# Performance work log

Measured on AMD Instinct MI355X. Metric: run time of the kernel, lower is better.

Reference implementation:

```python
import jax, jax.numpy as jnp
import numpy as np

D_MODEL = 1024
NUM_HEADS = 16
HEAD_DIM = D_MODEL // NUM_HEADS
SEQ_LEN = 2048
THETA = 10000.0


def setup_inputs() -> dict:
    key = jax.random.key(0)
    ks = jax.random.split(key, 9)
    s = 1.0 / np.sqrt(D_MODEL)
    inp = {
        "x": jax.random.normal(ks[0], (2, SEQ_LEN, D_MODEL), dtype=jnp.float32),
        "Wq": jax.random.uniform(ks[1], (D_MODEL, D_MODEL), jnp.float32, -s, s),
        "bq": jax.random.uniform(ks[2], (D_MODEL,), jnp.float32, -s, s),
        "Wk": jax.random.uniform(ks[3], (D_MODEL, D_MODEL), jnp.float32, -s, s),
        "bk": jax.random.uniform(ks[4], (D_MODEL,), jnp.float32, -s, s),
        "Wv": jax.random.uniform(ks[5], (D_MODEL, D_MODEL), jnp.float32, -s, s),
        "bv": jax.random.uniform(ks[6], (D_MODEL,), jnp.float32, -s, s),
        "Wo": jax.random.uniform(ks[7], (D_MODEL, D_MODEL), jnp.float32, -s, s),
        "bo": jax.random.uniform(ks[8], (D_MODEL,), jnp.float32, -s, s),
    }
    return inp


def _rope_cos_sin(seq_len, dim, theta):
    inv_freq = 1.0 / theta ** (jnp.arange(0, dim, 2, dtype=jnp.float32) / dim)  # [dim/2]
    t = jnp.arange(seq_len, dtype=jnp.float32)
    freqs = jnp.outer(t, inv_freq)  # [S, dim/2]
    return jnp.cos(freqs), jnp.sin(freqs)


def _apply_rope(x, cos, sin):
    # x: [B, H, S, head_dim]; interleaved complex pairs (even, odd)
    x2 = x.reshape(*x.shape[:-1], -1, 2)  # [B,H,S,hd/2,2]
    xe, xo = x2[..., 0], x2[..., 1]
    c = cos[None, None, :, :]
    s = sin[None, None, :, :]
    oe = xe * c - xo * s
    oo = xe * s + xo * c
    return jnp.stack([oe, oo], axis=-1).reshape(x.shape)


def reference(x, Wq, bq, Wk, bk, Wv, bv, Wo, bo):
    B, S, D = x.shape
    H, hd = NUM_HEADS, HEAD_DIM
    q = x @ Wq.T + bq
    k = x @ Wk.T + bk
    v = x @ Wv.T + bv
    # [B, H, S, hd]
    q = q.reshape(B, S, H, hd).transpose(0, 2, 1, 3)
    k = k.reshape(B, S, H, hd).transpose(0, 2, 1, 3)
    v = v.reshape(B, S, H, hd).transpose(0, 2, 1, 3)
    cos, sin = _rope_cos_sin(S, hd, THETA)
    q = _apply_rope(q, cos, sin)
    k = _apply_rope(k, cos, sin)
    scores = jnp.einsum("bhqd,bhkd->bhqk", q, k) / jnp.sqrt(jnp.float32(hd))
    causal = jnp.triu(jnp.ones((S, S), dtype=bool), k=1)
    scores = jnp.where(causal[None, None, :, :], -jnp.inf, scores)
    attn = jax.nn.softmax(scores, axis=-1)
    out = jnp.einsum("bhqk,bhkd->bhqd", attn, v)
    out = out.transpose(0, 2, 1, 3).reshape(B, S, D)
    return out @ Wo.T + bo
```

## Files before the change

kernel.cpp:

```cpp
#include <hip/hip_runtime.h>
#include <hip/hip_bf16.h>

#define S_LEN 2048
#define DM 1024
#define NH 16
#define HD 64
#define M_ROWS 4096
#define LOG2E 1.4426950408889634f
#define MASKVAL -1.0e4f
#define QSCALE 0.18033688011112042f

typedef __attribute__((ext_vector_type(8))) short short8;
typedef __attribute__((ext_vector_type(2))) float f32x2;
typedef __attribute__((ext_vector_type(4))) float f32x4;
typedef __attribute__((ext_vector_type(16))) float f32x16;

__device__ inline ushort f2b(float f) {
  union { float f; unsigned u; } v; v.f = f;
  unsigned r = v.u + 0x7fffu + ((v.u >> 16) & 1u);
  return (ushort)(r >> 16);
}

__device__ inline float b2f(ushort u) {
  union { unsigned u; float f; } v; v.u = ((unsigned)u) << 16; return v.f;
}

__device__ inline unsigned pk_bf16(float a, float b) {
  __hip_bfloat162 h = __float22bfloat162_rn(make_float2(a, b));
  union { __hip_bfloat162 h; unsigned u; } v; v.h = h;
  return v.u;
}

__device__ inline float fexp2(float x) { return __builtin_amdgcn_exp2f(x); }

__device__ inline void gl_lds16(const void* g, void* l) {
  __builtin_amdgcn_global_load_lds(
      (const __attribute__((address_space(1))) void*)g,
      (__attribute__((address_space(3))) void*)l, 16, 0, 0);
}

__global__ __launch_bounds__(256) void cast_rope_kernel(
    const float* __restrict__ x, const float* __restrict__ Wq, const float* __restrict__ Wk,
    const float* __restrict__ Wv, const float* __restrict__ Wo,
    ushort* __restrict__ xb, ushort* __restrict__ Wqb, ushort* __restrict__ Wkb,
    ushort* __restrict__ Wvb, ushort* __restrict__ Wob,
    float* __restrict__ ropeC, float* __restrict__ ropeS) {
  const int bid = blockIdx.x;
  if (bid >= 8192) {
    int idx = (bid - 8192) * 256 + threadIdx.x;
    int s = idx >> 5, i = idx & 31;
    float inv = exp2f(-(float)i * (13.287712379549449f / 32.0f));
    float a = (float)s * inv;
    ropeC[idx] = cosf(a);
    ropeS[idx] = sinf(a);
    return;
  }
  int i = bid * 256 + threadIdx.x;
  int r = i >> 18, off = i & 0x3FFFF;
  const float4* s;
  uint2* d;
  switch (r) {
    case 0: case 1: case 2: case 3: s = (const float4*)x + i;  d = (uint2*)xb + i;  break;
    case 4: s = (const float4*)Wq + off; d = (uint2*)Wqb + off; break;
    case 5: s = (const float4*)Wk + off; d = (uint2*)Wkb + off; break;
    case 6: s = (const float4*)Wv + off; d = (uint2*)Wvb + off; break;
    default: s = (const float4*)Wo + off; d = (uint2*)Wob + off; break;
  }
  float4 v = *s;
  uint2 o;
  o.x = pk_bf16(v.x, v.y);
  o.y = pk_bf16(v.z, v.w);
  *d = o;
}

__global__ __launch_bounds__(256) void gemm_qkv_kernel(const ushort* __restrict__ xb,
    const ushort* __restrict__ Wqb, const ushort* __restrict__ Wkb, const ushort* __restrict__ Wvb,
    const float* __restrict__ bq, const float* __restrict__ bk, const float* __restrict__ bv,
    const float* __restrict__ ropeC, const float* __restrict__ ropeS,
    ushort* __restrict__ qb, ushort* __restrict__ kb, ushort* __restrict__ vT) {
  __shared__ ushort lds[17408];
  ushort* As = lds;
  ushort* Bs = lds + 8192;
  const int z = blockIdx.z;
  const ushort* W = (z == 0) ? Wqb : ((z == 1) ? Wkb : Wvb);
  const float* bias = (z == 0) ? bq : ((z == 1) ? bk : bv);
  const int m0 = blockIdx.x * 128, n0 = blockIdx.y * 128;
  const int t = threadIdx.x, lane = t & 63, wave = t >> 6;
  const int wr = (wave >> 1) * 64, wc = (wave & 1) * 64;
  const int lr = lane & 15, lg = lane >> 4;

  const int slot0 = wave * 128 + lane, slot1 = slot0 + 64;
  const int row0 = slot0 >> 2, g0 = (slot0 & 3) ^ (row0 & 3);
  const int row1 = slot1 >> 2, g1 = (slot1 & 3) ^ (row1 & 3);
  const ushort* Ap0 = &xb[(size_t)(m0 + row0) * DM + g0 * 8];
  const ushort* Ap1 = &xb[(size_t)(m0 + row1) * DM + g1 * 8];
  const ushort* Wp0 = &W[(size_t)(n0 + row0) * DM + g0 * 8];
  const ushort* Wp1 = &W[(size_t)(n0 + row1) * DM + g1 * 8];

  f32x4 acc[4][4];
#pragma unroll
  for (int a = 0; a < 4; a++)
#pragma unroll
    for (int b = 0; b < 4; b++) acc[a][b] = (f32x4){0.f, 0.f, 0.f, 0.f};

  gl_lds16(Ap0, &As[slot0 * 8]);
  gl_lds16(Ap1, &As[slot1 * 8]);
  gl_lds16(Wp0, &Bs[slot0 * 8]);
  gl_lds16(Wp1, &Bs[slot1 * 8]);
  __syncthreads();

  int buf = 0;
  for (int i = 0; i < 32; i++) {
    if (i + 1 < 32) {
      const int k0 = (i + 1) * 32;
      const int bo = (buf ^ 1) * 4096;
      gl_lds16(Ap0 + k0, &As[bo + slot0 * 8]);
      gl_lds16(Ap1 + k0, &As[bo + slot1 * 8]);
      gl_lds16(Wp0 + k0, &Bs[bo + slot0 * 8]);
      gl_lds16(Wp1 + k0, &Bs[bo + slot1 * 8]);
    }
    const int fb = buf * 4096;
    short8 af[4], bf[4];
#pragma unroll
    for (int mt = 0; mt < 4; mt++) {
      const int row = wr + mt * 16 + lr;
      af[mt] = *(const short8*)&As[fb + (row * 4 + (lg ^ (row & 3))) * 8];
    }
#pragma unroll
    for (int nt = 0; nt < 4; nt++) {
      const int row = wc + nt * 16 + lr;
      bf[nt] = *(const short8*)&Bs[fb + (row * 4 + (lg ^ (row & 3))) * 8];
    }
#pragma unroll
    for (int mt = 0; mt < 4; mt++)
#pragma unroll
      for (int nt = 0; nt < 4; nt++)
        acc[mt][nt] = __builtin_amdgcn_mfma_f32_16x16x32_bf16(af[mt], bf[nt], acc[mt][nt], 0, 0, 0);
    __syncthreads();
    buf ^= 1;
  }

#pragma unroll
  for (int mt = 0; mt < 4; mt++) {
#pragma unroll
    for (int nt = 0; nt < 4; nt++) {
      const int nloc = wc + nt * 16 + lr;
      const float bn = bias[n0 + nloc];
#pragma unroll
      for (int r = 0; r < 4; r++) {
        const int mloc = wr + mt * 16 + lg * 4 + r;
        const ushort v = f2b(acc[mt][nt][r] + bn);
        if (z < 2) lds[mloc * 136 + nloc] = v;
        else       lds[nloc * 136 + mloc] = v;
      }
    }
  }
  __syncthreads();

  const int b = m0 >> 11;
  if (z < 2) {
    ushort* dst = (z == 0) ? qb : kb;
    const float qscale = (z == 0) ? QSCALE : 1.0f;
#pragma unroll
    for (int c = 0; c < 8; c++) {
      const int sloc = c * 16 + (t >> 4);
      const int nloc = (t & 15) * 8;
      short8 val = *(const short8*)&lds[sloc * 136 + nloc];
      const int s = (m0 + sloc) & (S_LEN - 1);
      const int h = (n0 + nloc) >> 6;
      const int d0 = nloc & 63;
      const float4 cv = *(const float4*)&ropeC[s * 32 + d0 / 2];
      const float4 sv = *(const float4*)&ropeS[s * 32 + d0 / 2];
      uint4 o;
      {
        float e = b2f((ushort)val[0]), od = b2f((ushort)val[1]);
        o.x = pk_bf16((e * cv.x - od * sv.x) * qscale, (e * sv.x + od * cv.x) * qscale);
      }
      {
        float e = b2f((ushort)val[2]), od = b2f((ushort)val[3]);
        o.y = pk_bf16((e * cv.y - od * sv.y) * qscale, (e * sv.y + od * cv.y) * qscale);
      }
      {
        float e = b2f((ushort)val[4]), od = b2f((ushort)val[5]);
        o.z = pk_bf16((e * cv.z - od * sv.z) * qscale, (e * sv.z + od * cv.z) * qscale);
      }
      {
        float e = b2f((ushort)val[6]), od = b2f((ushort)val[7]);
        o.w = pk_bf16((e * cv.w - od * sv.w) * qscale, (e * sv.w + od * cv.w) * qscale);
      }
      *(uint4*)&dst[(((size_t)b * NH + h) * S_LEN + s) * HD + d0] = o;
    }
  } else {
    const int sbase = m0 & (S_LEN - 1);
#pragma unroll
    for (int c = 0; c < 8; c++) {
      const int nloc = c * 16 + (t >> 4);
      const int s0 = (t & 15) * 8;
      short8 val = *(const short8*)&lds[nloc * 136 + s0];
      const int h = (n0 + nloc) >> 6;
      const int d = nloc & 63;
      *(short8*)&vT[(((size_t)b * NH + h) * HD + d) * S_LEN + sbase + s0] = val;
    }
  }
}

__global__ __launch_bounds__(256) void flash_kernel(const ushort* __restrict__ qb,
                                                    const ushort* __restrict__ kb,
                                                    const ushort* __restrict__ vT,
                                                    ushort* __restrict__ Oh,
                                                    float* __restrict__ lsum) {
  __shared__ ushort lds[24576];
  const int t = threadIdx.x, lane = t & 63, wave = t >> 6;
  const int q31 = lane & 31, h = lane >> 5;
  const int bh = blockIdx.y;
  const int cid = blockIdx.x;
  const int g = (cid >= 24) ? 3 : (cid >= 12) ? 2 : (cid >= 4) ? 1 : 0;
  const int nc = g + 1;
  const int o = cid - 4 * ((g * (g + 1)) >> 1);
  const int qi = o / nc;
  const int c = o - qi * nc;
  const int qt = g * 4 + qi;
  const int q0 = qt * 128;
  const int ntiles = 2 * qt + 2;
  const int kstart = c * 8;
  const int kend = min(kstart + 8, ntiles);
  const int pidx = bh * 40 + cid;

  const ushort* kbh = kb + (size_t)bh * S_LEN * HD;
  const ushort* vbh = vT + (size_t)bh * HD * S_LEN;

  const int qrow = q0 + wave * 32 + q31;
  const ushort* qptr = qb + ((size_t)bh * S_LEN + qrow) * HD + h * 8;
  short8 qf[4];
#pragma unroll
  for (int s = 0; s < 4; s++) qf[s] = *(const short8*)(qptr + s * 16);

  const int slot0 = wave * 128 + lane, slot1 = slot0 + 64;
  const int row0 = slot0 >> 3, g0 = (slot0 & 7) ^ (row0 & 7);
  const int row1 = slot1 >> 3, g1 = (slot1 & 7) ^ (row1 & 7);
  const int lo0 = wave * 128 * 8, lo1 = lo0 + 64 * 8;

  int foff[4][2];
#pragma unroll
  for (int s = 0; s < 4; s++)
#pragma unroll
    for (int st = 0; st < 2; st++) {
      const int row = st * 32 + q31;
      foff[s][st] = (row * 8 + ((2 * s + h) ^ (row & 7))) * 8;
    }

  const ushort* kp0 = kbh + (size_t)(kstart * 64 + row0) * HD + g0 * 8;
  const ushort* kp1 = kbh + (size_t)(kstart * 64 + row1) * HD + g1 * 8;
  const ushort* vp0 = vbh + (size_t)row0 * S_LEN + kstart * 64 + g0 * 8;
  const ushort* vp1 = vbh + (size_t)row1 * S_LEN + kstart * 64 + g1 * 8;
  gl_lds16(kp0, &lds[lo0]);
  gl_lds16(kp1, &lds[lo1]);
  gl_lds16(vp0, &lds[12288 + lo0]);
  gl_lds16(vp1, &lds[12288 + lo1]);
  kp0 += 64 * HD; kp1 += 64 * HD; vp0 += 64; vp1 += 64;
  gl_lds16(kp0, &lds[4096 + lo0]);
  gl_lds16(kp1, &lds[4096 + lo1]);
  gl_lds16(vp0, &lds[16384 + lo0]);
  gl_lds16(vp1, &lds[16384 + lo1]);
  kp0 += 64 * HD; kp1 += 64 * HD; vp0 += 64; vp1 += 64;

  f32x16 O[2];
#pragma unroll
  for (int st = 0; st < 2; st++)
#pragma unroll
    for (int r = 0; r < 16; r++) O[st][r] = 0.f;

  f32x16 zc;
#pragma unroll
  for (int r = 0; r < 16; r++) zc[r] = 0.f;

  f32x2 lpA = (f32x2){0.f, 0.f}, lpB = (f32x2){0.f, 0.f};

  asm volatile("s_waitcnt vmcnt(4)" ::: "memory");
  __builtin_amdgcn_s_barrier();
  __builtin_amdgcn_sched_barrier(0);

  int cur = 0;
  for (int kt = kstart; kt < kend; ++kt) {
    const bool pref = (kt + 2 < kend);
    if (pref) {
      const int nb = (cur >= 1) ? cur - 1 : 2;
      const int ko = nb * 4096, vo = 12288 + nb * 4096;
      gl_lds16(kp0, &lds[ko + lo0]);
      gl_lds16(kp1, &lds[ko + lo1]);
      gl_lds16(vp0, &lds[vo + lo0]);
      gl_lds16(vp1, &lds[vo + lo1]);
      kp0 += 64 * HD; kp1 += 64 * HD; vp0 += 64; vp1 += 64;
    }
    const ushort* Kb = &lds[cur * 4096];
    const ushort* Vb = &lds[12288 + cur * 4096];

    f32x16 sc0, sc1;
    __builtin_amdgcn_s_setprio(1);
    sc0 = __builtin_amdgcn_mfma_f32_32x32x16_bf16(
        *(const short8*)&Kb[foff[0][0]], qf[0], zc, 0, 0, 0);
    sc1 = __builtin_amdgcn_mfma_f32_32x32x16_bf16(
        *(const short8*)&Kb[foff[0][1]], qf[0], zc, 0, 0, 0);
#pragma unroll
    for (int s = 1; s < 4; s++) {
      sc0 = __builtin_amdgcn_mfma_f32_32x32x16_bf16(
          *(const short8*)&Kb[foff[s][0]], qf[s], sc0, 0, 0, 0);
      sc1 = __builtin_amdgcn_mfma_f32_32x32x16_bf16(
          *(const short8*)&Kb[foff[s][1]], qf[s], sc1, 0, 0, 0);
    }
    __builtin_amdgcn_s_setprio(0);

    if (kt * 64 + 63 > q0 + wave * 32) {
#pragma unroll
      for (int r = 0; r < 16; r++) {
        const int kc0 = kt * 64 + (r & 3) + 8 * (r >> 2) + 4 * h;
        if (kc0 > qrow) sc0[r] = MASKVAL;
        if (kc0 + 32 > qrow) sc1[r] = MASKVAL;
      }
    }
#pragma unroll
    for (int r = 0; r < 16; r += 2) {
      const float a0 = fexp2(sc0[r]), a1 = fexp2(sc0[r + 1]);
      const float b0 = fexp2(sc1[r]), b1 = fexp2(sc1[r + 1]);
      sc0[r] = a0; sc0[r + 1] = a1;
      sc1[r] = b0; sc1[r + 1] = b1;
      lpA += (f32x2){a0, a1};
      lpB += (f32x2){b0, b1};
    }

    unsigned pp[8][2];
#pragma unroll
    for (int rg = 0; rg < 4; rg++) {
      pp[rg][0] = pk_bf16(sc0[4 * rg + 0], sc0[4 * rg + 1]);
      pp[rg][1] = pk_bf16(sc0[4 * rg + 2], sc0[4 * rg + 3]);
      pp[4 + rg][0] = pk_bf16(sc1[4 * rg + 0], sc1[4 * rg + 1]);
      pp[4 + rg][1] = pk_bf16(sc1[4 * rg + 2], sc1[4 * rg + 3]);
    }
    __builtin_amdgcn_s_setprio(1);
#pragma unroll
    for (int s = 0; s < 4; s++) {
      unsigned d0 = pp[2 * s][0], e0 = pp[2 * s + 1][0];
      unsigned d1 = pp[2 * s][1], e1 = pp[2 * s + 1][1];
      asm("v_permlane32_swap_b32 %0, %1" : "+v"(d0), "+v"(e0));
      asm("v_permlane32_swap_b32 %0, %1" : "+v"(d1), "+v"(e1));
      union { unsigned u[4]; short8 v; } pf;
      pf.u[0] = d0;
      pf.u[1] = d1;
      pf.u[2] = e0;
      pf.u[3] = e1;
      O[0] = __builtin_amdgcn_mfma_f32_32x32x16_bf16(
          *(const short8*)&Vb[foff[s][0]], pf.v, O[0], 0, 0, 0);
      O[1] = __builtin_amdgcn_mfma_f32_32x32x16_bf16(
          *(const short8*)&Vb[foff[s][1]], pf.v, O[1], 0, 0, 0);
    }
    __builtin_amdgcn_s_setprio(0);

    if (kt + 1 < kend) {
      if (pref) asm volatile("s_waitcnt vmcnt(4)" ::: "memory");
      else      asm volatile("s_waitcnt vmcnt(0)" ::: "memory");
      __builtin_amdgcn_s_barrier();
      __builtin_amdgcn_sched_barrier(0);
    }
    cur = (cur >= 2) ? 0 : cur + 1;
  }

  float lacc = (lpA[0] + lpA[1]) + (lpB[0] + lpB[1]);
  lacc += __shfl_xor(lacc, 32);

  ushort* obase = Oh + ((size_t)pidx * 128 + wave * 32 + q31) * HD;
#pragma unroll
  for (int st = 0; st < 2; st++)
#pragma unroll
    for (int rg = 0; rg < 4; rg++) {
      const int d0 = st * 32 + 8 * rg + 4 * h;
      uint2 w;
      w.x = pk_bf16(O[st][4 * rg + 0], O[st][4 * rg + 1]);
      w.y = pk_bf16(O[st][4 * rg + 2], O[st][4 * rg + 3]);
      *(uint2*)&obase[d0] = w;
    }
  if (h == 0) lsum[(size_t)pidx * 128 + wave * 32 + q31] = lacc;
}

__global__ __launch_bounds__(256) void combine_kernel(const ushort* __restrict__ Oh,
                                                      const float* __restrict__ lsum,
                                                      ushort* __restrict__ attn) {
  const int tid = blockIdx.x * 256 + threadIdx.x;
  const int d8 = tid & 7;
  const int q = (tid >> 3) & (S_LEN - 1);
  const int bh = tid >> 14;
  const int qt = q >> 7, row = q & 127;
  const int g = qt >> 2, nc = g + 1;
  const int base = 4 * ((g * (g + 1)) >> 1) + (qt & 3) * nc;
  const int p0 = bh * 40 + base;

  float l = 0.f;
  float acc[8];
#pragma unroll
  for (int j = 0; j < 8; j++) acc[j] = 0.f;
  for (int c = 0; c < nc; c++) {
    const size_t rowidx = (size_t)(p0 + c) * 128 + row;
    l += lsum[rowidx];
    const uint4 a = *(const uint4*)&Oh[rowidx * HD + d8 * 8];
    const unsigned au[4] = {a.x, a.y, a.z, a.w};
#pragma unroll
    for (int j = 0; j < 4; j++) {
      acc[2 * j] += b2f((ushort)(au[j] & 0xffff));
      acc[2 * j + 1] += b2f((ushort)(au[j] >> 16));
    }
  }
  const float inv = 1.f / l;
  uint4 o;
  unsigned* op = (unsigned*)&o;
#pragma unroll
  for (int j = 0; j < 4; j++) op[j] = pk_bf16(acc[2 * j] * inv, acc[2 * j + 1] * inv);
  const int b = bh >> 4, hh = bh & 15;
  *(uint4*)&attn[((size_t)b * S_LEN + q) * DM + hh * HD + d8 * 8] = o;
}

__global__ __launch_bounds__(256) void gemm_out_kernel(const ushort* __restrict__ attn,
                                                       const ushort* __restrict__ Wob,
                                                       const float* __restrict__ bo,
                                                       float* __restrict__ out) {
  __shared__ ushort As[2][4096];
  __shared__ ushort Bs[2][2048];
  const int m0 = blockIdx.x * 128, n0 = blockIdx.y * 64;
  const int t = threadIdx.x, lane = t & 63, wave = t >> 6;
  const int wm = (wave >> 1) * 64, wn = (wave & 1) * 32;
  const int lr = lane & 15, lg = lane >> 4;
  const int slotA0 = wave * 128 + lane, slotA1 = slotA0 + 64;
  const int rowA0 = slotA0 >> 2, gA0 = (slotA0 & 3) ^ (rowA0 & 3);
  const int rowA1 = slotA1 >> 2, gA1 = (slotA1 & 3) ^ (rowA1 & 3);
  const int slotB = wave * 64 + lane;
  const int rowB = slotB >> 2, gB = (slotB & 3) ^ (rowB & 3);
  const ushort* Ap0 = &attn[(size_t)(m0 + rowA0) * DM + gA0 * 8];
  const ushort* Ap1 = &attn[(size_t)(m0 + rowA1) * DM + gA1 * 8];
  const ushort* Wp  = &Wob[(size_t)(n0 + rowB) * DM + gB * 8];

  f32x4 acc[4][2];
#pragma unroll
  for (int a = 0; a < 4; a++)
#pragma unroll
    for (int b = 0; b < 2; b++) acc[a][b] = (f32x4){0.f, 0.f, 0.f, 0.f};

  gl_lds16(Ap0, &As[0][slotA0 * 8]);
  gl_lds16(Ap1, &As[0][slotA1 * 8]);
  gl_lds16(Wp, &Bs[0][slotB * 8]);
  __syncthreads();

  int buf = 0;
  for (int i = 0; i < 32; i++) {
    if (i + 1 < 32) {
      const int k0 = (i + 1) * 32;
      gl_lds16(Ap0 + k0, &As[buf ^ 1][slotA0 * 8]);
      gl_lds16(Ap1 + k0, &As[buf ^ 1][slotA1 * 8]);
      gl_lds16(Wp + k0, &Bs[buf ^ 1][slotB * 8]);
    }
    short8 af[4], bf[2];
#pragma unroll
    for (int mt = 0; mt < 4; mt++) {
      const int row = wm + mt * 16 + lr;
      af[mt] = *(const short8*)&As[buf][(row * 4 + (lg ^ (row & 3))) * 8];
    }
#pragma unroll
    for (int nt = 0; nt < 2; nt++) {
      const int row = wn + nt * 16 + lr;
      bf[nt] = *(const short8*)&Bs[buf][(row * 4 + (lg ^ (row & 3))) * 8];
    }
#pragma unroll
    for (int mt = 0; mt < 4; mt++)
#pragma unroll
      for (int nt = 0; nt < 2; nt++)
        acc[mt][nt] = __builtin_amdgcn_mfma_f32_16x16x32_bf16(af[mt], bf[nt], acc[mt][nt], 0, 0, 0);
    __syncthreads();
    buf ^= 1;
  }

#pragma unroll
  for (int mt = 0; mt < 4; mt++) {
#pragma unroll
    for (int nt = 0; nt < 2; nt++) {
      const int n = n0 + wn + nt * 16 + lr;
      const float bn = bo[n];
#pragma unroll
      for (int r = 0; r < 4; r++) {
        const int m = m0 + wm + mt * 16 + lg * 4 + r;
        out[(size_t)m * DM + n] = acc[mt][nt][r] + bn;
      }
    }
  }
}

extern "C" void kernel_launch(void* const* d_in, const int* in_sizes, int n_in,
                              void* d_out, int out_size, void* d_ws, size_t ws_size,
                              hipStream_t stream) {
  const float* x  = (const float*)d_in[0];
  const float* Wq = (const float*)d_in[1];
  const float* bq = (const float*)d_in[2];
  const float* Wk = (const float*)d_in[3];
  const float* bk = (const float*)d_in[4];
  const float* Wv = (const float*)d_in[5];
  const float* bv = (const float*)d_in[6];
  const float* Wo = (const float*)d_in[7];
  const float* bo = (const float*)d_in[8];
  float* out = (float*)d_out;

  char* ws = (char*)d_ws;
  size_t off = 0;
  auto alloc = [&](size_t bytes) { char* p = ws + off; off += (bytes + 255) & ~255ull; return p; };
  ushort* xb   = (ushort*)alloc((size_t)M_ROWS * DM * 2);
  ushort* Wqb  = (ushort*)alloc((size_t)DM * DM * 2);
  ushort* Wkb  = (ushort*)alloc((size_t)DM * DM * 2);
  ushort* Wvb  = (ushort*)alloc((size_t)DM * DM * 2);
  ushort* Wob  = (ushort*)alloc((size_t)DM * DM * 2);
  ushort* qb   = (ushort*)alloc((size_t)M_ROWS * DM * 2);
  ushort* kb   = (ushort*)alloc((size_t)M_ROWS * DM * 2);
  ushort* vTb  = (ushort*)alloc((size_t)M_ROWS * DM * 2);
  ushort* attn = (ushort*)alloc((size_t)M_ROWS * DM * 2);
  ushort* Ohb  = (ushort*)alloc((size_t)1280 * 128 * HD * 2);
  float* lsb   = (float*)alloc((size_t)1280 * 128 * 4);
  float* ropeC = (float*)alloc((size_t)S_LEN * 32 * 4);
  float* ropeS = (float*)alloc((size_t)S_LEN * 32 * 4);
  (void)ws_size; (void)in_sizes; (void)n_in; (void)out_size;

  cast_rope_kernel<<<8448, 256, 0, stream>>>(x, Wq, Wk, Wv, Wo, xb, Wqb, Wkb, Wvb, Wob,
                                             ropeC, ropeS);
  gemm_qkv_kernel<<<dim3(M_ROWS / 128, DM / 128, 3), 256, 0, stream>>>(
      xb, Wqb, Wkb, Wvb, bq, bk, bv, ropeC, ropeS, qb, kb, vTb);
  flash_kernel<<<dim3(40, 32), 256, 0, stream>>>(qb, kb, vTb, Ohb, lsb);
  combine_kernel<<<2048, 256, 0, stream>>>(Ohb, lsb, attn);
  gemm_out_kernel<<<dim3(M_ROWS / 128, DM / 64), 256, 0, stream>>>(attn, Wob, bo, out);
}
```

Measured before the change: 193.7 us.

## Triple-buffer GEMM loads with single barrier and XCD-aware block swizzle

Both GEMM kernels move from double-buffered LDS staging with two syncthreads per k-step to a three-stage ring. Loads run two iterations ahead, with an explicit vmcnt wait and one barrier per step. Block indices in the GEMMs and the flash kernel are remapped so blocks landing on the same XCD (id mod 8) get neighbouring tiles, which should improve L2 reuse. The cost is more LDS per block, which may reduce occupancy, and waitcnt logic that is easy to get wrong.

```diff
diff --git a/kernel.cpp b/kernel.cpp
--- a/kernel.cpp
+++ b/kernel.cpp
@@ -78,13 +78,14 @@
     const float* __restrict__ bq, const float* __restrict__ bk, const float* __restrict__ bv,
     const float* __restrict__ ropeC, const float* __restrict__ ropeS,
     ushort* __restrict__ qb, ushort* __restrict__ kb, ushort* __restrict__ vT) {
-  __shared__ ushort lds[17408];
-  ushort* As = lds;
-  ushort* Bs = lds + 8192;
-  const int z = blockIdx.z;
+  __shared__ ushort lds[24576];
+  const int lid = blockIdx.x;
+  const int swz = (lid & 7) * 96 + (lid >> 3);
+  const int z = swz >> 8;
+  const int rem = swz & 255;
+  const int m0 = (rem & 31) * 128, n0 = (rem >> 5) * 128;
   const ushort* W = (z == 0) ? Wqb : ((z == 1) ? Wkb : Wvb);
   const float* bias = (z == 0) ? bq : ((z == 1) ? bk : bv);
-  const int m0 = blockIdx.x * 128, n0 = blockIdx.y * 128;
   const int t = threadIdx.x, lane = t & 63, wave = t >> 6;
   const int wr = (wave >> 1) * 64, wc = (wave & 1) * 64;
   const int lr = lane & 15, lg = lane >> 4;
@@ -103,42 +104,55 @@
 #pragma unroll
     for (int b = 0; b < 4; b++) acc[a][b] = (f32x4){0.f, 0.f, 0.f, 0.f};
 
-  gl_lds16(Ap0, &As[slot0 * 8]);
-  gl_lds16(Ap1, &As[slot1 * 8]);
-  gl_lds16(Wp0, &Bs[slot0 * 8]);
-  gl_lds16(Wp1, &Bs[slot1 * 8]);
-  __syncthreads();
-
-  int buf = 0;
+  gl_lds16(Ap0, &lds[slot0 * 8]);
+  gl_lds16(Ap1, &lds[slot1 * 8]);
+  gl_lds16(Wp0, &lds[12288 + slot0 * 8]);
+  gl_lds16(Wp1, &lds[12288 + slot1 * 8]);
+  gl_lds16(Ap0 + 32, &lds[4096 + slot0 * 8]);
+  gl_lds16(Ap1 + 32, &lds[4096 + slot1 * 8]);
+  gl_lds16(Wp0 + 32, &lds[16384 + slot0 * 8]);
+  gl_lds16(Wp1 + 32, &lds[16384 + slot1 * 8]);
+  asm volatile("s_waitcnt vmcnt(4)" ::: "memory");
+  __builtin_amdgcn_s_barrier();
+  __builtin_amdgcn_sched_barrier(0);
+
+  int cur = 0;
   for (int i = 0; i < 32; i++) {
-    if (i + 1 < 32) {
-      const int k0 = (i + 1) * 32;
-      const int bo = (buf ^ 1) * 4096;
-      gl_lds16(Ap0 + k0, &As[bo + slot0 * 8]);
-      gl_lds16(Ap1 + k0, &As[bo + slot1 * 8]);
-      gl_lds16(Wp0 + k0, &Bs[bo + slot0 * 8]);
-      gl_lds16(Wp1 + k0, &Bs[bo + slot1 * 8]);
-    }
-    const int fb = buf * 4096;
+    const bool pref = (i + 2 < 32);
+    if (pref) {
+      const int nb = (cur >= 1) ? cur - 1 : 2;
+      const int k0 = (i + 2) * 32;
+      gl_lds16(Ap0 + k0, &lds[nb * 4096 + slot0 * 8]);
+      gl_lds16(Ap1 + k0, &lds[nb * 4096 + slot1 * 8]);
+      gl_lds16(Wp0 + k0, &lds[12288 + nb * 4096 + slot0 * 8]);
+      gl_lds16(Wp1 + k0, &lds[12288 + nb * 4096 + slot1 * 8]);
+    }
+    const int fb = cur * 4096;
     short8 af[4], bf[4];
 #pragma unroll
     for (int mt = 0; mt < 4; mt++) {
       const int row = wr + mt * 16 + lr;
-      af[mt] = *(const short8*)&As[fb + (row * 4 + (lg ^ (row & 3))) * 8];
+      af[mt] = *(const short8*)&lds[fb + (row * 4 + (lg ^ (row & 3))) * 8];
     }
 #pragma unroll
     for (int nt = 0; nt < 4; nt++) {
       const int row = wc + nt * 16 + lr;
-      bf[nt] = *(const short8*)&Bs[fb + (row * 4 + (lg ^ (row & 3))) * 8];
+      bf[nt] = *(const short8*)&lds[12288 + fb + (row * 4 + (lg ^ (row & 3))) * 8];
     }
 #pragma unroll
     for (int mt = 0; mt < 4; mt++)
 #pragma unroll
       for (int nt = 0; nt < 4; nt++)
         acc[mt][nt] = __builtin_amdgcn_mfma_f32_16x16x32_bf16(af[mt], bf[nt], acc[mt][nt], 0, 0, 0);
-    __syncthreads();
-    buf ^= 1;
-  }
+    if (i + 1 < 32) {
+      if (pref) asm volatile("s_waitcnt vmcnt(4)" ::: "memory");
+      else      asm volatile("s_waitcnt vmcnt(0)" ::: "memory");
+      __builtin_amdgcn_s_barrier();
+      __builtin_amdgcn_sched_barrier(0);
+    }
+    cur = (cur >= 2) ? 0 : cur + 1;
+  }
+  __syncthreads();
 
 #pragma unroll
   for (int mt = 0; mt < 4; mt++) {
@@ -212,8 +226,10 @@
   __shared__ ushort lds[24576];
   const int t = threadIdx.x, lane = t & 63, wave = t >> 6;
   const int q31 = lane & 31, h = lane >> 5;
-  const int bh = blockIdx.y;
-  const int cid = blockIdx.x;
+  const int lid = blockIdx.x + 40 * blockIdx.y;
+  const int swz = (lid & 7) * 160 + (lid >> 3);
+  const int bh = swz / 40;
+  const int cid = swz - bh * 40;
   const int g = (cid >= 24) ? 3 : (cid >= 12) ? 2 : (cid >= 4) ? 1 : 0;
   const int nc = g + 1;
   const int o = cid - 4 * ((g * (g + 1)) >> 1);
@@ -421,9 +437,10 @@
                                                        const ushort* __restrict__ Wob,
                                                        const float* __restrict__ bo,
                                                        float* __restrict__ out) {
-  __shared__ ushort As[2][4096];
-  __shared__ ushort Bs[2][2048];
-  const int m0 = blockIdx.x * 128, n0 = blockIdx.y * 64;
+  __shared__ ushort lds[18432];
+  const int lid = blockIdx.x;
+  const int swz = (lid & 7) * 64 + (lid >> 3);
+  const int m0 = (swz & 31) * 128, n0 = (swz >> 5) * 64;
   const int t = threadIdx.x, lane = t & 63, wave = t >> 6;
   const int wm = (wave >> 1) * 64, wn = (wave & 1) * 32;
   const int lr = lane & 15, lg = lane >> 4;
@@ -442,37 +459,49 @@
 #pragma unroll
     for (int b = 0; b < 2; b++) acc[a][b] = (f32x4){0.f, 0.f, 0.f, 0.f};
 
-  gl_lds16(Ap0, &As[0][slotA0 * 8]);
-  gl_lds16(Ap1, &As[0][slotA1 * 8]);
-  gl_lds16(Wp, &Bs[0][slotB * 8]);
-  __syncthreads();
-
-  int buf = 0;
+  gl_lds16(Ap0, &lds[slotA0 * 8]);
+  gl_lds16(Ap1, &lds[slotA1 * 8]);
+  gl_lds16(Wp, &lds[12288 + slotB * 8]);
+  gl_lds16(Ap0 + 32, &lds[4096 + slotA0 * 8]);
+  gl_lds16(Ap1 + 32, &lds[4096 + slotA1 * 8]);
+  gl_lds16(Wp + 32, &lds[14336 + slotB * 8]);
+  asm volatile("s_waitcnt vmcnt(3)" ::: "memory");
+  __builtin_amdgcn_s_barrier();
+  __builtin_amdgcn_sched_barrier(0);
+
+  int cur = 0;
   for (int i = 0; i < 32; i++) {
-    if (i + 1 < 32) {
-      const int k0 = (i + 1) * 32;
-      gl_lds16(Ap0 + k0, &As[buf ^ 1][slotA0 * 8]);
-      gl_lds16(Ap1 + k0, &As[buf ^ 1][slotA1 * 8]);
-      gl_lds16(Wp + k0, &Bs[buf ^ 1][slotB * 8]);
+    const bool pref = (i + 2 < 32);
+    if (pref) {
+      const int nb = (cur >= 1) ? cur - 1 : 2;
+      const int k0 = (i + 2) * 32;
+      gl_lds16(Ap0 + k0, &lds[nb * 4096 + slotA0 * 8]);
+      gl_lds16(Ap1 + k0, &lds[nb * 4096 + slotA1 * 8]);
+      gl_lds16(Wp + k0, &lds[12288 + nb * 2048 + slotB * 8]);
     }
     short8 af[4], bf[2];
 #pragma unroll
     for (int mt = 0; mt < 4; mt++) {
       const int row = wm + mt * 16 + lr;
-      af[mt] = *(const short8*)&As[buf][(row * 4 + (lg ^ (row & 3))) * 8];
+      af[mt] = *(const short8*)&lds[cur * 4096 + (row * 4 + (lg ^ (row & 3))) * 8];
     }
 #pragma unroll
     for (int nt = 0; nt < 2; nt++) {
       const int row = wn + nt * 16 + lr;
-      bf[nt] = *(const short8*)&Bs[buf][(row * 4 + (lg ^ (row & 3))) * 8];
+      bf[nt] = *(const short8*)&lds[12288 + cur * 2048 + (row * 4 + (lg ^ (row & 3))) * 8];
     }
 #pragma unroll
     for (int mt = 0; mt < 4; mt++)
 #pragma unroll
       for (int nt = 0; nt < 2; nt++)
         acc[mt][nt] = __builtin_amdgcn_mfma_f32_16x16x32_bf16(af[mt], bf[nt], acc[mt][nt], 0, 0, 0);
-    __syncthreads();
-    buf ^= 1;
+    if (i + 1 < 32) {
+      if (pref) asm volatile("s_waitcnt vmcnt(3)" ::: "memory");
+      else      asm volatile("s_waitcnt vmcnt(0)" ::: "memory");
+      __builtin_amdgcn_s_barrier();
+      __builtin_amdgcn_sched_barrier(0);
+    }
+    cur = (cur >= 2) ? 0 : cur + 1;
   }
 
 #pragma unroll
@@ -524,9 +553,9 @@
 
   cast_rope_kernel<<<8448, 256, 0, stream>>>(x, Wq, Wk, Wv, Wo, xb, Wqb, Wkb, Wvb, Wob,
                                              ropeC, ropeS);
-  gemm_qkv_kernel<<<dim3(M_ROWS / 128, DM / 128, 3), 256, 0, stream>>>(
+  gemm_qkv_kernel<<<768, 256, 0, stream>>>(
       xb, Wqb, Wkb, Wvb, bq, bk, bv, ropeC, ropeS, qb, kb, vTb);
   flash_kernel<<<dim3(40, 32), 256, 0, stream>>>(qb, kb, vTb, Ohb, lsb);
   combine_kernel<<<2048, 256, 0, stream>>>(Ohb, lsb, attn);
-  gemm_out_kernel<<<dim3(M_ROWS / 128, DM / 64), 256, 0, stream>>>(attn, Wob, bo, out);
-}
+  gemm_out_kernel<<<512, 256, 0, stream>>>(attn, Wob, bo, out);
+}
```

New measurement: 193.5 us. Within noise of the previous version (-0.1%).
